# Kernel optimization log

Measured on AMD Instinct MI355X. Metric: run time of the kernel, lower is better.

## Reference

```python
import jax, jax.numpy as jnp
import numpy as np

N_NODES = 50000
N_EDGES = 500000
IN_F, HID, EMB = 128, 256, 128

def setup_inputs() -> dict:
    key = jax.random.key(0)
    ks = jax.random.split(key, 9)
    x = jax.random.normal(ks[0], (N_NODES, IN_F), dtype=jnp.float32)
    src = jax.random.randint(ks[1], (N_EDGES,), 0, N_NODES, dtype=jnp.int32)
    dst = jax.random.randint(ks[2], (N_EDGES,), 0, N_NODES, dtype=jnp.int32)
    def lin(k, fan_in, fan_out):
        bound = 1.0 / np.sqrt(fan_in)
        kw, kb = jax.random.split(k)
        W = jax.random.uniform(kw, (fan_in, fan_out), minval=-bound, maxval=bound, dtype=jnp.float32)
        b = jax.random.uniform(kb, (fan_out,), minval=-bound, maxval=bound, dtype=jnp.float32)
        return W, b
    W1, b1 = lin(ks[3], IN_F, HID)
    W2, b2 = lin(ks[4], HID, HID)
    W3, b3 = lin(ks[5], HID, EMB)
    return {"x": x, "src": src, "dst": dst, "W1": W1, "b1": b1,
            "W2": W2, "b2": b2, "W3": W3, "b3": b3}

def _gcn_layer(h, src, dst, W, b):
    # sum messages from src nodes into dst nodes, then linear
    agg = jax.ops.segment_sum(h[src], dst, num_segments=N_NODES)  # [N, F]
    return agg @ W + b

def reference(x, src, dst, W1, b1, W2, b2, W3, b3):
    h = jax.nn.relu(_gcn_layer(x, src, dst, W1, b1))
    h = jax.nn.relu(_gcn_layer(h, src, dst, W2, b2))
    h = _gcn_layer(h, src, dst, W3, b3)
    # dgl.mean_nodes on a single graph: mean of relu(h) over all nodes -> [EMB]
    return jnp.mean(jax.nn.relu(h), axis=0)
```

## Files before the change

kernel.cpp:

```cpp
#include <hip/hip_runtime.h>

#define N_NODES 50000
#define N_EDGES 500000

typedef __attribute__((ext_vector_type(8))) short short8;
typedef __attribute__((ext_vector_type(8))) unsigned short ushort8v;
typedef __attribute__((ext_vector_type(4))) float floatx4;
typedef __attribute__((ext_vector_type(4))) unsigned int uint4v;

__device__ inline float bf2f(unsigned short u) {
    unsigned int x = ((unsigned int)u) << 16;
    return __builtin_bit_cast(float, x);
}
__device__ inline unsigned short f2bf(float f) {
    unsigned int x = __builtin_bit_cast(unsigned int, f);
    x += 0x7fff + ((x >> 16) & 1);
    return (unsigned short)(x >> 16);
}

__device__ __forceinline__ void gld_lds16(const unsigned short* g, unsigned short* l) {
    __builtin_amdgcn_global_load_lds((const __attribute__((address_space(1))) void*)g,
                                     (__attribute__((address_space(3))) void*)l, 16, 0, 0);
}

__device__ inline void accum16B(float2* a, ushort8v rv) {
    uint4v u = __builtin_bit_cast(uint4v, rv);
    #pragma unroll
    for (int p = 0; p < 4; p++) {
        float lo = __builtin_bit_cast(float, u[p] << 16);
        float hi = __builtin_bit_cast(float, u[p] & 0xFFFF0000u);
        a[p].x += lo;
        a[p].y += hi;
    }
}


__global__ void scan_block_kernel(const int* __restrict__ deg, int* __restrict__ partial,
                                  int* __restrict__ bsum, int n) {
    __shared__ int s[256];
    int i = blockIdx.x * 256 + threadIdx.x;
    int v = (i < n) ? deg[i] : 0;
    s[threadIdx.x] = v;
    __syncthreads();
    #pragma unroll
    for (int d = 1; d < 256; d <<= 1) {
        int t = (threadIdx.x >= d) ? s[threadIdx.x - d] : 0;
        __syncthreads();
        s[threadIdx.x] += t;
        __syncthreads();
    }
    if (i < n) partial[i] = s[threadIdx.x];
    if (threadIdx.x == 255) bsum[blockIdx.x] = s[255];
}

__global__ __launch_bounds__(256) void finalize_kernel(const int* __restrict__ partial,
                                                       const int* __restrict__ bsum,
                                                       int* __restrict__ cur,
                                                       int* __restrict__ off, int n) {
    __shared__ int sr[256];
    int t = threadIdx.x;
    sr[t] = (t < blockIdx.x) ? bsum[t] : 0;
    __syncthreads();
    #pragma unroll
    for (int d = 128; d > 0; d >>= 1) {
        if (t < d) sr[t] += sr[t + d];
        __syncthreads();
    }
    int base = sr[0];
    int i = blockIdx.x * 256 + t;
    if (i == 0) off[0] = 0;
    if (i < n) {
        int incl = base + partial[i];
        off[i + 1] = incl;
        cur[i] = incl - cur[i];
    }
}

__global__ void fill_kernel(const int* __restrict__ src, const int* __restrict__ dst,
                            int* __restrict__ cur, int* __restrict__ csr, int nE) {
    int e = blockIdx.x * 256 + threadIdx.x;
    if (e < nE) {
        int p = atomicAdd(&cur[dst[e]], 1);
        csr[p] = src[e];
    }
}


__global__ __launch_bounds__(256) void histprep_kernel(const int* __restrict__ dst,
                                                       int* __restrict__ deg,
                                                       const float* __restrict__ W1,
                                                       const float* __restrict__ W2,
                                                       const float* __restrict__ W3,
                                                       const float* __restrict__ x,
                                                       unsigned short* __restrict__ Wt1,
                                                       unsigned short* __restrict__ Wt2,
                                                       unsigned short* __restrict__ Wt3,
                                                       unsigned short* __restrict__ xb) {
    int idx = blockIdx.x * 256 + threadIdx.x;
    if (idx < N_EDGES) { atomicAdd(&deg[dst[idx]], 1); return; }
    idx -= N_EDGES;
    if (idx < 32768) {
        int k = idx >> 8, n = idx & 255;
        Wt1[n * 128 + k] = f2bf(W1[idx]);
    } else if (idx < 98304) {
        int i = idx - 32768;
        int k = i >> 8, n = i & 255;
        Wt2[n * 256 + k] = f2bf(W2[i]);
    } else if (idx < 131072) {
        int i = idx - 98304;
        int k = i >> 7, n = i & 127;
        Wt3[n * 256 + k] = f2bf(W3[i]);
    } else {
        int i = (idx - 131072) * 4;
        if (i < N_NODES * 128) {
            float4 v = *(const float4*)(x + i);
            ushort4 o;
            o.x = f2bf(v.x); o.y = f2bf(v.y); o.z = f2bf(v.z); o.w = f2bf(v.w);
            *(ushort4*)(xb + i) = o;
        }
    }
}


__global__ __launch_bounds__(256) void agg256_kernel(const unsigned short* __restrict__ h,
                                                     const int* __restrict__ off,
                                                     const int* __restrict__ csr,
                                                     unsigned short* __restrict__ outp) {
    int wave = threadIdx.x >> 6, lane = threadIdx.x & 63;
    int node = blockIdx.x * 4 + wave;
    int half = lane >> 5;
    int f0 = (lane & 31) * 8;
    int s = __builtin_amdgcn_readfirstlane(off[node]);
    int e = __builtin_amdgcn_readfirstlane(off[node + 1]);
    float2 a[4];
    #pragma unroll
    for (int p = 0; p < 4; p++) a[p] = make_float2(0.f, 0.f);
    int i = s;
    for (; i + 8 <= e; i += 8) {
        ushort8v r[4];
        #pragma unroll
        for (int j = 0; j < 4; j++) {
            int i0 = csr[i + 2 * j];
            int i1 = csr[i + 2 * j + 1];
            int id = half ? i1 : i0;
            r[j] = *(const ushort8v*)(h + (size_t)id * 256 + f0);
        }
        #pragma unroll
        for (int j = 0; j < 4; j++) accum16B(a, r[j]);
    }
    int rem = e - i;
    if (rem > 0) {
        int nr = (rem + 1) >> 1;
        ushort8v r[4];
        #pragma unroll
        for (int j = 0; j < 4; j++) {
            if (j < nr) {
                int b0 = i + 2 * j, b1 = b0 + 1;
                int i0 = csr[b0];
                int i1 = csr[b1 < e ? b1 : e - 1];
                int id = half ? i1 : i0;
                r[j] = *(const ushort8v*)(h + (size_t)id * 256 + f0);
            }
        }
        #pragma unroll
        for (int j = 0; j < 4; j++) {
            if (j < nr && (i + 2 * j + half) < e) accum16B(a, r[j]);
        }
    }
    #pragma unroll
    for (int p = 0; p < 4; p++) {
        a[p].x += __shfl_xor(a[p].x, 32, 64);
        a[p].y += __shfl_xor(a[p].y, 32, 64);
    }
    if (half == 0) {
        ushort8v o;
        #pragma unroll
        for (int p = 0; p < 4; p++) { o[2 * p] = f2bf(a[p].x); o[2 * p + 1] = f2bf(a[p].y); }
        *(ushort8v*)(outp + (size_t)node * 256 + f0) = o;
    }
}


__device__ inline void agg128_body(const unsigned short* __restrict__ h,
                                   const int* __restrict__ off,
                                   const int* __restrict__ csr,
                                   int node, int quad, int f0, float2* a) {
    int s = __builtin_amdgcn_readfirstlane(off[node]);
    int e = __builtin_amdgcn_readfirstlane(off[node + 1]);
    int i = s;
    for (; i + 8 <= e; i += 8) {
        ushort8v r[2];
        #pragma unroll
        for (int j = 0; j < 2; j++) {
            int base = i + 4 * j;
            int i0 = csr[base], i1 = csr[base + 1], i2 = csr[base + 2], i3 = csr[base + 3];
            int id = quad == 0 ? i0 : quad == 1 ? i1 : quad == 2 ? i2 : i3;
            r[j] = *(const ushort8v*)(h + (size_t)id * 128 + f0);
        }
        #pragma unroll
        for (int j = 0; j < 2; j++) accum16B(a, r[j]);
    }
    int rem = e - i;
    if (rem > 0) {
        int nr = (rem + 3) >> 2;
        ushort8v r[2];
        #pragma unroll
        for (int j = 0; j < 2; j++) {
            if (j < nr) {
                int base = i + 4 * j;
                int c1 = base + 1 < e ? base + 1 : e - 1;
                int c2 = base + 2 < e ? base + 2 : e - 1;
                int c3 = base + 3 < e ? base + 3 : e - 1;
                int i0 = csr[base], i1 = csr[c1], i2 = csr[c2], i3 = csr[c3];
                int id = quad == 0 ? i0 : quad == 1 ? i1 : quad == 2 ? i2 : i3;
                r[j] = *(const ushort8v*)(h + (size_t)id * 128 + f0);
            }
        }
        #pragma unroll
        for (int j = 0; j < 2; j++) {
            if (j < nr && (i + 4 * j + quad) < e) accum16B(a, r[j]);
        }
    }
    #pragma unroll
    for (int p = 0; p < 4; p++) {
        a[p].x += __shfl_xor(a[p].x, 16, 64);
        a[p].y += __shfl_xor(a[p].y, 16, 64);
        a[p].x += __shfl_xor(a[p].x, 32, 64);
        a[p].y += __shfl_xor(a[p].y, 32, 64);
    }
}

__global__ __launch_bounds__(256) void agg128_kernel(const unsigned short* __restrict__ h,
                                                     const int* __restrict__ off,
                                                     const int* __restrict__ csr,
                                                     unsigned short* __restrict__ outp) {
    int wave = threadIdx.x >> 6, lane = threadIdx.x & 63;
    int node = blockIdx.x * 4 + wave;
    int quad = lane >> 4;
    int f0 = (lane & 15) * 8;
    float2 a[4];
    #pragma unroll
    for (int p = 0; p < 4; p++) a[p] = make_float2(0.f, 0.f);
    agg128_body(h, off, csr, node, quad, f0, a);
    if (quad == 0) {
        ushort8v o;
        #pragma unroll
        for (int p = 0; p < 4; p++) { o[2 * p] = f2bf(a[p].x); o[2 * p + 1] = f2bf(a[p].y); }
        *(ushort8v*)(outp + (size_t)node * 128 + f0) = o;
    }
}


__global__ __launch_bounds__(256) void agg3_mean_kernel(const unsigned short* __restrict__ t,
                                                        const int* __restrict__ off,
                                                        const int* __restrict__ csr,
                                                        const float* __restrict__ b3,
                                                        float* __restrict__ partial) {
    __shared__ float sm[4 * 128];
    int wave = threadIdx.x >> 6, lane = threadIdx.x & 63;
    int node = blockIdx.x * 4 + wave;
    int quad = lane >> 4;
    int f0 = (lane & 15) * 8;
    float2 a[4];
    #pragma unroll
    for (int p = 0; p < 4; p++) a[p] = make_float2(0.f, 0.f);
    agg128_body(t, off, csr, node, quad, f0, a);
    if (quad == 0) {
        #pragma unroll
        for (int p = 0; p < 4; p++) {
            sm[wave * 128 + f0 + 2 * p]     = fmaxf(a[p].x + b3[f0 + 2 * p], 0.f);
            sm[wave * 128 + f0 + 2 * p + 1] = fmaxf(a[p].y + b3[f0 + 2 * p + 1], 0.f);
        }
    }
    __syncthreads();
    if (threadIdx.x < 128) {
        int f = threadIdx.x;
        float p = sm[f] + sm[128 + f] + sm[256 + f] + sm[384 + f];
        partial[(size_t)blockIdx.x * 128 + f] = p;
    }
}

__global__ __launch_bounds__(256) void mean_reduce_kernel(const float* __restrict__ partial,
                                                          float* __restrict__ outp, int nRows) {
    __shared__ float s[256];
    int f = threadIdx.x & 127, half = threadIdx.x >> 7;
    int chunk = (nRows + gridDim.x - 1) / gridDim.x;
    int r0 = blockIdx.x * chunk;
    int r1 = r0 + chunk < nRows ? r0 + chunk : nRows;
    float acc = 0.f;
    for (int r = r0 + half; r < r1; r += 2) acc += partial[(size_t)r * 128 + f];
    s[threadIdx.x] = acc;
    __syncthreads();
    if (half == 0) atomicAdd(&outp[f], (s[f] + s[f + 128]) * (1.0f / N_NODES));
}


template<typename T> __device__ inline void storeC(T* p, float v);
template<> __device__ inline void storeC<float>(float* p, float v) { *p = v; }
template<> __device__ inline void storeC<unsigned short>(unsigned short* p, float v) { *p = f2bf(v); }

template<int BN, typename OUT_T>
__global__ __launch_bounds__(2 * BN) void gemm_bf16_kernel(const unsigned short* __restrict__ A,
                                                           const unsigned short* __restrict__ Bt,
                                                           const float* __restrict__ bias,
                                                           OUT_T* __restrict__ C,
                                                           int M, int K, int N, int doRelu) {
    constexpr int BM = 128, BK = 32;
    constexpr int T = 2 * BN;
    __shared__ unsigned short As[BM * BK];
    __shared__ unsigned short Bs[BN * BK];
    int tid = threadIdx.x;
    int m0 = blockIdx.y * BM, n0 = blockIdx.x * BN;
    int wave = tid >> 6, lane = tid & 63;
    int wm = wave & 1, wn = wave >> 1;
    int mlane = lane & 15, kgrp = lane >> 4;

    floatx4 acc[4][4];
    #pragma unroll
    for (int i = 0; i < 4; i++)
        #pragma unroll
        for (int j = 0; j < 4; j++) acc[i][j] = (floatx4){0.f, 0.f, 0.f, 0.f};

    for (int k0 = 0; k0 < K; k0 += BK) {
        #pragma unroll
        for (int c = tid; c < BM * 4; c += T) {
            int r = c >> 2, cb = (c & 3) * 8;
            gld_lds16(A + (size_t)(m0 + r) * K + k0 + cb, &As[c * 8]);
        }
        #pragma unroll
        for (int c = tid; c < BN * 4; c += T) {
            int r = c >> 2, cb = (c & 3) * 8;
            gld_lds16(Bt + (size_t)(n0 + r) * K + k0 + cb, &Bs[c * 8]);
        }
        __syncthreads();
        short8 af[4], bfr[4];
        #pragma unroll
        for (int mt = 0; mt < 4; mt++)
            af[mt] = *(const short8*)&As[(wm * 64 + mt * 16 + mlane) * BK + kgrp * 8];
        #pragma unroll
        for (int nt = 0; nt < 4; nt++)
            bfr[nt] = *(const short8*)&Bs[(wn * 64 + nt * 16 + mlane) * BK + kgrp * 8];
        #pragma unroll
        for (int mt = 0; mt < 4; mt++)
            #pragma unroll
            for (int nt = 0; nt < 4; nt++)
                acc[mt][nt] = __builtin_amdgcn_mfma_f32_16x16x32_bf16(af[mt], bfr[nt],
                                                                      acc[mt][nt], 0, 0, 0);
        __syncthreads();
    }
    #pragma unroll
    for (int mt = 0; mt < 4; mt++) {
        #pragma unroll
        for (int nt = 0; nt < 4; nt++) {
            int col = n0 + wn * 64 + nt * 16 + mlane;
            float bv = bias ? bias[col] : 0.f;
            #pragma unroll
            for (int r = 0; r < 4; r++) {
                int row = m0 + wm * 64 + mt * 16 + kgrp * 4 + r;
                if (row < M) {
                    float v = acc[mt][nt][r] + bv;
                    if (doRelu) v = fmaxf(v, 0.f);
                    storeC(C + (size_t)row * N + col, v);
                }
            }
        }
    }
}


extern "C" void kernel_launch(void* const* d_in, const int* in_sizes, int n_in,
                              void* d_out, int out_size, void* d_ws, size_t ws_size,
                              hipStream_t stream) {
    const float* x   = (const float*)d_in[0];
    const int*   src = (const int*)d_in[1];
    const int*   dst = (const int*)d_in[2];
    const float* W1 = (const float*)d_in[3];
    const float* b1 = (const float*)d_in[4];
    const float* W2 = (const float*)d_in[5];
    const float* b2 = (const float*)d_in[6];
    const float* W3 = (const float*)d_in[7];
    const float* b3 = (const float*)d_in[8];
    float* out = (float*)d_out;

    char* ws = (char*)d_ws;
    size_t o = 0;
    auto alloc = [&](size_t bytes) -> char* {
        char* p = ws + o;
        o = (o + bytes + 255) & ~(size_t)255;
        return p;
    };
    int* off     = (int*)alloc((size_t)(N_NODES + 1) * 4);
    int* cur     = (int*)alloc((size_t)N_NODES * 4);
    int* csrIdx  = (int*)alloc((size_t)N_EDGES * 4);
    int* partial = (int*)alloc((size_t)N_NODES * 4);
    int* bsum    = (int*)alloc(256 * 4);
    unsigned short* Wt1 = (unsigned short*)alloc((size_t)128 * 256 * 2);
    unsigned short* Wt2 = (unsigned short*)alloc((size_t)256 * 256 * 2);
    unsigned short* Wt3 = (unsigned short*)alloc((size_t)256 * 128 * 2);
    char* R1 = alloc((size_t)N_NODES * 256 * 2);
    char* R2 = alloc((size_t)N_NODES * 256 * 2);
    char* R3 = alloc((size_t)N_NODES * 256 * 2);
    (void)alloc(65536);

    unsigned short* xb    = (unsigned short*)R1;
    unsigned short* aggX  = (unsigned short*)R2;
    unsigned short* h1    = (unsigned short*)R3;
    unsigned short* agg2o = (unsigned short*)R1;
    unsigned short* h2    = (unsigned short*)R2;
    unsigned short* t     = (unsigned short*)R3;
    float*          pmean = (float*)R1;

    const int nb = (N_NODES + 255) / 256;

    hipMemsetAsync(cur, 0, (size_t)N_NODES * 4, stream);
    const int hpThreads = N_EDGES + 131072 + N_NODES * 128 / 4;
    histprep_kernel<<<(hpThreads + 255) / 256, 256, 0, stream>>>(dst, cur, W1, W2, W3, x,
                                                                 Wt1, Wt2, Wt3, xb);
    scan_block_kernel<<<nb, 256, 0, stream>>>(cur, partial, bsum, N_NODES);
    finalize_kernel<<<nb, 256, 0, stream>>>(partial, bsum, cur, off, N_NODES);
    fill_kernel<<<(N_EDGES + 255) / 256, 256, 0, stream>>>(src, dst, cur, csrIdx, N_EDGES);

    const int mb = (N_NODES + 127) / 128;

    agg128_kernel<<<N_NODES / 4, 256, 0, stream>>>(xb, off, csrIdx, aggX);
    gemm_bf16_kernel<256, unsigned short><<<dim3(1, mb), 512, 0, stream>>>(aggX, Wt1, b1, h1,
                                                                           N_NODES, 128, 256, 1);
    agg256_kernel<<<N_NODES / 4, 256, 0, stream>>>(h1, off, csrIdx, agg2o);
    gemm_bf16_kernel<256, unsigned short><<<dim3(1, mb), 512, 0, stream>>>(agg2o, Wt2, b2, h2,
                                                                           N_NODES, 256, 256, 1);
    gemm_bf16_kernel<128, unsigned short><<<dim3(1, mb), 256, 0, stream>>>(h2, Wt3, nullptr, t,
                                                                           N_NODES, 256, 128, 0);
    agg3_mean_kernel<<<N_NODES / 4, 256, 0, stream>>>(t, off, csrIdx, b3, pmean);

    hipMemsetAsync(out, 0, 128 * 4, stream);
    mean_reduce_kernel<<<128, 256, 0, stream>>>(pmean, out, N_NODES / 4);
}
```

Baseline: 300.5 us.

## Merge scan kernels into one-pass decoupled scan and shrink GEMM tiles

Replaces the two-kernel block scan plus finalize with a single kernel. Each block publishes its sum through a flag-encoded atomic and spin-waits on the sums of earlier blocks. The zeroing of the block sums and the output is folded into the existing prep kernel, which removes a memset and a launch. The GEMM moves from a 128xBN tile with up to 512 threads to a 64x128 tile with 256 threads, giving more blocks for occupancy. The spin-wait relies on all earlier blocks being resident or scheduled first, which is a forward-progress assumption.

```diff
diff --git a/kernel.cpp b/kernel.cpp
--- a/kernel.cpp
+++ b/kernel.cpp
@@ -31,57 +31,6 @@
         float hi = __builtin_bit_cast(float, u[p] & 0xFFFF0000u);
         a[p].x += lo;
         a[p].y += hi;
-    }
-}
-
-
-__global__ void scan_block_kernel(const int* __restrict__ deg, int* __restrict__ partial,
-                                  int* __restrict__ bsum, int n) {
-    __shared__ int s[256];
-    int i = blockIdx.x * 256 + threadIdx.x;
-    int v = (i < n) ? deg[i] : 0;
-    s[threadIdx.x] = v;
-    __syncthreads();
-    #pragma unroll
-    for (int d = 1; d < 256; d <<= 1) {
-        int t = (threadIdx.x >= d) ? s[threadIdx.x - d] : 0;
-        __syncthreads();
-        s[threadIdx.x] += t;
-        __syncthreads();
-    }
-    if (i < n) partial[i] = s[threadIdx.x];
-    if (threadIdx.x == 255) bsum[blockIdx.x] = s[255];
-}
-
-__global__ __launch_bounds__(256) void finalize_kernel(const int* __restrict__ partial,
-                                                       const int* __restrict__ bsum,
-                                                       int* __restrict__ cur,
-                                                       int* __restrict__ off, int n) {
-    __shared__ int sr[256];
-    int t = threadIdx.x;
-    sr[t] = (t < blockIdx.x) ? bsum[t] : 0;
-    __syncthreads();
-    #pragma unroll
-    for (int d = 128; d > 0; d >>= 1) {
-        if (t < d) sr[t] += sr[t + d];
-        __syncthreads();
-    }
-    int base = sr[0];
-    int i = blockIdx.x * 256 + t;
-    if (i == 0) off[0] = 0;
-    if (i < n) {
-        int incl = base + partial[i];
-        off[i + 1] = incl;
-        cur[i] = incl - cur[i];
-    }
-}
-
-__global__ void fill_kernel(const int* __restrict__ src, const int* __restrict__ dst,
-                            int* __restrict__ cur, int* __restrict__ csr, int nE) {
-    int e = blockIdx.x * 256 + threadIdx.x;
-    if (e < nE) {
-        int p = atomicAdd(&cur[dst[e]], 1);
-        csr[p] = src[e];
     }
 }
 
@@ -95,11 +44,15 @@
                                                        unsigned short* __restrict__ Wt1,
                                                        unsigned short* __restrict__ Wt2,
                                                        unsigned short* __restrict__ Wt3,
-                                                       unsigned short* __restrict__ xb) {
+                                                       unsigned short* __restrict__ xb,
+                                                       int* __restrict__ bsum,
+                                                       float* __restrict__ outZ) {
     int idx = blockIdx.x * 256 + threadIdx.x;
     if (idx < N_EDGES) { atomicAdd(&deg[dst[idx]], 1); return; }
     idx -= N_EDGES;
     if (idx < 32768) {
+        if (idx < 256) bsum[idx] = 0;
+        if (idx < 128) outZ[idx] = 0.f;
         int k = idx >> 8, n = idx & 255;
         Wt1[n * 128 + k] = f2bf(W1[idx]);
     } else if (idx < 98304) {
@@ -122,6 +75,58 @@
 }
 
 
+__global__ __launch_bounds__(256) void scan_onepass_kernel(int* __restrict__ cur,
+                                                           int* __restrict__ bsum,
+                                                           int* __restrict__ off, int n) {
+    __shared__ int s[256];
+    int b = blockIdx.x, t = threadIdx.x;
+    int i = b * 256 + t;
+    int v = (i < n) ? cur[i] : 0;
+    s[t] = v;
+    __syncthreads();
+    #pragma unroll
+    for (int d = 1; d < 256; d <<= 1) {
+        int u = (t >= d) ? s[t - d] : 0;
+        __syncthreads();
+        s[t] += u;
+        __syncthreads();
+    }
+    int incl = s[t];
+    if (t == 255) atomicExch(&bsum[b], s[255] + 1);
+    int pre = 0;
+    if (t < b) {
+        volatile int* p = (volatile int*)&bsum[t];
+        int vv;
+        while ((vv = *p) == 0) { }
+        pre = vv - 1;
+    }
+    __syncthreads();
+    s[t] = pre;
+    __syncthreads();
+    #pragma unroll
+    for (int d = 128; d > 0; d >>= 1) {
+        if (t < d) s[t] += s[t + d];
+        __syncthreads();
+    }
+    int base = s[0];
+    if (i == 0) off[0] = 0;
+    if (i < n) {
+        int inclG = base + incl;
+        off[i + 1] = inclG;
+        cur[i] = inclG - v;
+    }
+}
+
+__global__ void fill_kernel(const int* __restrict__ src, const int* __restrict__ dst,
+                            int* __restrict__ cur, int* __restrict__ csr, int nE) {
+    int e = blockIdx.x * 256 + threadIdx.x;
+    if (e < nE) {
+        int p = atomicAdd(&cur[dst[e]], 1);
+        csr[p] = src[e];
+    }
+}
+
+
 __global__ __launch_bounds__(256) void agg256_kernel(const unsigned short* __restrict__ h,
                                                      const int* __restrict__ off,
                                                      const int* __restrict__ csr,
@@ -299,49 +304,49 @@
 template<> __device__ inline void storeC<float>(float* p, float v) { *p = v; }
 template<> __device__ inline void storeC<unsigned short>(unsigned short* p, float v) { *p = f2bf(v); }
 
-template<int BN, typename OUT_T>
-__global__ __launch_bounds__(2 * BN) void gemm_bf16_kernel(const unsigned short* __restrict__ A,
-                                                           const unsigned short* __restrict__ Bt,
-                                                           const float* __restrict__ bias,
-                                                           OUT_T* __restrict__ C,
-                                                           int M, int K, int N, int doRelu) {
-    constexpr int BM = 128, BK = 32;
-    constexpr int T = 2 * BN;
+template<typename OUT_T>
+__global__ __launch_bounds__(256) void gemm_bf16_kernel(const unsigned short* __restrict__ A,
+                                                        const unsigned short* __restrict__ Bt,
+                                                        const float* __restrict__ bias,
+                                                        OUT_T* __restrict__ C,
+                                                        int M, int K, int N, int doRelu) {
+    constexpr int BM = 64, BN = 128, BK = 32;
     __shared__ unsigned short As[BM * BK];
     __shared__ unsigned short Bs[BN * BK];
     int tid = threadIdx.x;
     int m0 = blockIdx.y * BM, n0 = blockIdx.x * BN;
     int wave = tid >> 6, lane = tid & 63;
-    int wm = wave & 1, wn = wave >> 1;
+    int wm = wave >> 1, wn = wave & 1;
     int mlane = lane & 15, kgrp = lane >> 4;
 
-    floatx4 acc[4][4];
-    #pragma unroll
-    for (int i = 0; i < 4; i++)
+    floatx4 acc[2][4];
+    #pragma unroll
+    for (int i = 0; i < 2; i++)
         #pragma unroll
         for (int j = 0; j < 4; j++) acc[i][j] = (floatx4){0.f, 0.f, 0.f, 0.f};
 
     for (int k0 = 0; k0 < K; k0 += BK) {
-        #pragma unroll
-        for (int c = tid; c < BM * 4; c += T) {
+        {
+            int c = tid;
             int r = c >> 2, cb = (c & 3) * 8;
             gld_lds16(A + (size_t)(m0 + r) * K + k0 + cb, &As[c * 8]);
         }
         #pragma unroll
-        for (int c = tid; c < BN * 4; c += T) {
+        for (int it = 0; it < 2; it++) {
+            int c = tid + it * 256;
             int r = c >> 2, cb = (c & 3) * 8;
             gld_lds16(Bt + (size_t)(n0 + r) * K + k0 + cb, &Bs[c * 8]);
         }
         __syncthreads();
-        short8 af[4], bfr[4];
-        #pragma unroll
-        for (int mt = 0; mt < 4; mt++)
-            af[mt] = *(const short8*)&As[(wm * 64 + mt * 16 + mlane) * BK + kgrp * 8];
+        short8 af[2], bfr[4];
+        #pragma unroll
+        for (int mt = 0; mt < 2; mt++)
+            af[mt] = *(const short8*)&As[(wm * 32 + mt * 16 + mlane) * BK + kgrp * 8];
         #pragma unroll
         for (int nt = 0; nt < 4; nt++)
             bfr[nt] = *(const short8*)&Bs[(wn * 64 + nt * 16 + mlane) * BK + kgrp * 8];
         #pragma unroll
-        for (int mt = 0; mt < 4; mt++)
+        for (int mt = 0; mt < 2; mt++)
             #pragma unroll
             for (int nt = 0; nt < 4; nt++)
                 acc[mt][nt] = __builtin_amdgcn_mfma_f32_16x16x32_bf16(af[mt], bfr[nt],
@@ -349,14 +354,14 @@
         __syncthreads();
     }
     #pragma unroll
-    for (int mt = 0; mt < 4; mt++) {
+    for (int mt = 0; mt < 2; mt++) {
         #pragma unroll
         for (int nt = 0; nt < 4; nt++) {
             int col = n0 + wn * 64 + nt * 16 + mlane;
             float bv = bias ? bias[col] : 0.f;
             #pragma unroll
             for (int r = 0; r < 4; r++) {
-                int row = m0 + wm * 64 + mt * 16 + kgrp * 4 + r;
+                int row = m0 + wm * 32 + mt * 16 + kgrp * 4 + r;
                 if (row < M) {
                     float v = acc[mt][nt][r] + bv;
                     if (doRelu) v = fmaxf(v, 0.f);
@@ -392,7 +397,6 @@
     int* off     = (int*)alloc((size_t)(N_NODES + 1) * 4);
     int* cur     = (int*)alloc((size_t)N_NODES * 4);
     int* csrIdx  = (int*)alloc((size_t)N_EDGES * 4);
-    int* partial = (int*)alloc((size_t)N_NODES * 4);
     int* bsum    = (int*)alloc(256 * 4);
     unsigned short* Wt1 = (unsigned short*)alloc((size_t)128 * 256 * 2);
     unsigned short* Wt2 = (unsigned short*)alloc((size_t)256 * 256 * 2);
@@ -415,23 +419,20 @@
     hipMemsetAsync(cur, 0, (size_t)N_NODES * 4, stream);
     const int hpThreads = N_EDGES + 131072 + N_NODES * 128 / 4;
     histprep_kernel<<<(hpThreads + 255) / 256, 256, 0, stream>>>(dst, cur, W1, W2, W3, x,
-                                                                 Wt1, Wt2, Wt3, xb);
-    scan_block_kernel<<<nb, 256, 0, stream>>>(cur, partial, bsum, N_NODES);
-    finalize_kernel<<<nb, 256, 0, stream>>>(partial, bsum, cur, off, N_NODES);
+                                                                 Wt1, Wt2, Wt3, xb, bsum, out);
+    scan_onepass_kernel<<<nb, 256, 0, stream>>>(cur, bsum, off, N_NODES);
     fill_kernel<<<(N_EDGES + 255) / 256, 256, 0, stream>>>(src, dst, cur, csrIdx, N_EDGES);
 
-    const int mb = (N_NODES + 127) / 128;
+    const int mb = (N_NODES + 63) / 64;
 
     agg128_kernel<<<N_NODES / 4, 256, 0, stream>>>(xb, off, csrIdx, aggX);
-    gemm_bf16_kernel<256, unsigned short><<<dim3(1, mb), 512, 0, stream>>>(aggX, Wt1, b1, h1,
-                                                                           N_NODES, 128, 256, 1);
+    gemm_bf16_kernel<unsigned short><<<dim3(2, mb), 256, 0, stream>>>(aggX, Wt1, b1, h1,
+                                                                      N_NODES, 128, 256, 1);
     agg256_kernel<<<N_NODES / 4, 256, 0, stream>>>(h1, off, csrIdx, agg2o);
-    gemm_bf16_kernel<256, unsigned short><<<dim3(1, mb), 512, 0, stream>>>(agg2o, Wt2, b2, h2,
-                                                                           N_NODES, 256, 256, 1);
-    gemm_bf16_kernel<128, unsigned short><<<dim3(1, mb), 256, 0, stream>>>(h2, Wt3, nullptr, t,
-                                                                           N_NODES, 256, 128, 0);
+    gemm_bf16_kernel<unsigned short><<<dim3(2, mb), 256, 0, stream>>>(agg2o, Wt2, b2, h2,
+                                                                      N_NODES, 256, 256, 1);
+    gemm_bf16_kernel<unsigned short><<<dim3(1, mb), 256, 0, stream>>>(h2, Wt3, nullptr, t,
+                                                                      N_NODES, 256, 128, 0);
     agg3_mean_kernel<<<N_NODES / 4, 256, 0, stream>>>(t, off, csrIdx, b3, pmean);
-
-    hipMemsetAsync(out, 0, 128 * 4, stream);
     mean_reduce_kernel<<<128, 256, 0, stream>>>(pmean, out, N_NODES / 4);
 }
```

New measurement: 299.4 us. Within noise of the previous version (-0.4%).
